# Kernel optimization log

Hardware: AMD Instinct MI355X
Metric: run time of the kernel (lower is better)

Reference implementation:

```python
import jax, jax.numpy as jnp
import numpy as np

D = 128  # hard-coded hidden dim in MLP_T

def setup_inputs() -> dict:
    key = jax.random.key(0)
    ks = jax.random.split(key, 8)
    N, IN = 16384, 768
    return {
        "x": jax.random.normal(ks[0], (N, IN), dtype=jnp.float32),
        "decay_value": 1,
        "W_token": jax.random.normal(ks[1], (IN, D), dtype=jnp.float32) * (IN ** -0.5),
        "b_token": jax.random.normal(ks[2], (D,), dtype=jnp.float32) * 0.02,
        "W_qkv": jax.random.normal(ks[3], (D, 3 * D), dtype=jnp.float32) * (D ** -0.5),
        "b_qkv": jax.random.normal(ks[4], (3 * D,), dtype=jnp.float32) * 0.02,
        "W_fc": jax.random.normal(ks[5], (D, 1), dtype=jnp.float32) * (D ** -0.5),
        "b_fc": jax.random.normal(ks[6], (1,), dtype=jnp.float32) * 0.02,
    }

def reference(x, decay_value, W_token, b_token, W_qkv, b_qkv, W_fc, b_fc):
    # token projection: [N, in_chan] -> [N, 128]
    h = x @ W_token + b_token
    # qkv: [N, 384] split along feature dim into q, k, v of [N, 128]
    qkv = h @ W_qkv + b_qkv
    q, k, v = qkv[:, :D], qkv[:, D:2 * D], qkv[:, 2 * D:]
    # sigmoid attention (no row normalization); dropout is identity in eval mode
    att_scores = jax.nn.sigmoid(q @ k.T)            # [N, N]
    att = att_scores @ v                            # [N, 128]
    out = att @ W_fc + b_fc                         # [N, 1]
    # GradientReversal is identity in the forward pass
    return out
```

## Files before the change

kernel.cpp:

```cpp
#include <hip/hip_runtime.h>
#include <hip/hip_bf16.h>
#include <stdint.h>

#define N_ROWS 16384

typedef __bf16 bf16x8 __attribute__((ext_vector_type(8)));
typedef float f32x4 __attribute__((ext_vector_type(4)));

#define AS1 __attribute__((address_space(1)))
#define AS3 __attribute__((address_space(3)))

#define OFF_WCS  0u
#define OFF_BC   589824u
#define OFF_QB   591360u
#define OFF_KB   4785664u
#define OFF_WV   8979968u

__global__ void prep(const float* __restrict__ Wt, const float* __restrict__ Wq,
                     const float* __restrict__ bt, const float* __restrict__ bq,
                     __bf16* __restrict__ WcS, float* __restrict__ bc) {
    int u = blockIdx.x * 256 + threadIdx.x;
    if (u < 768 * 96) {
        int k = u / 96, n4 = u % 96;
        float s[4] = {0, 0, 0, 0};
        const float* wtp = Wt + k * 128;
        const float* wqp = Wq + n4 * 4;
#pragma unroll 8
        for (int d = 0; d < 128; d++) {
            float a = wtp[d];
            float4 b = *(const float4*)(wqp + d * 384);
            s[0] += a * b.x; s[1] += a * b.y; s[2] += a * b.z; s[3] += a * b.w;
        }
        int kb_ = k >> 6, c = (k >> 3) & 7, k7 = k & 7;
#pragma unroll
        for (int j = 0; j < 4; j++) {
            int n = n4 * 4 + j;
            WcS[n * 768 + kb_ * 64 + ((c ^ (n & 7)) << 3) + k7] = (__bf16)s[j];
        }
    }
    if (u < 384) {
        float s = bq[u];
        for (int d = 0; d < 128; d++) s += bt[d] * Wq[d * 384 + u];
        bc[u] = s;
    }
}

__launch_bounds__(256)
__global__ void gemm_qkv(const float* __restrict__ x, const __bf16* __restrict__ WcS,
                         const float* __restrict__ bc, const float* __restrict__ W_fc,
                         const float* __restrict__ b_fc,
                         __bf16* __restrict__ qb, __bf16* __restrict__ kb,
                         float* __restrict__ wv, float* __restrict__ out) {
    __shared__ float  Asm_[64 * 64];
    __shared__ __bf16 Bsm[128 * 64];
    __shared__ float  wred[64];
    const int tid = threadIdx.x, wave = tid >> 6, lane = tid & 63;
    const int n16 = lane & 15, q = lane >> 4;
    const int mh = wave >> 1, nw = wave & 1;
    const int row0 = blockIdx.x * 64;
    const int sp = blockIdx.y;

    if (sp == 2 && tid < 64) out[row0 + tid] = b_fc[0];

    const char* aptr[4];
    const char* bptr[4];
    {
        int p = (lane & 15) >> 1, half = lane & 1;
#pragma unroll
        for (int i = 0; i < 4; i++) {
            int ar = row0 + wave * 16 + i * 4 + (lane >> 4);
            aptr[i] = (const char*)x + (size_t)ar * 3072 + ((p ^ (ar & 7)) * 8 + half * 4) * 4;
            int br = sp * 128 + wave * 32 + i * 8 + (lane >> 3);
            bptr[i] = (const char*)WcS + (size_t)br * 1536 + (lane & 7) * 16;
        }
    }
    f32x4 acc[2][4];
#pragma unroll
    for (int mt = 0; mt < 2; mt++)
#pragma unroll
        for (int t = 0; t < 4; t++) acc[mt][t] = (f32x4){0, 0, 0, 0};

    for (int kbi = 0; kbi < 12; kbi++) {
#pragma unroll
        for (int i = 0; i < 4; i++)
            __builtin_amdgcn_global_load_lds((const AS1 void*)(aptr[i] + kbi * 256),
                (AS3 void*)((char*)Asm_ + wave * 4096 + i * 1024), 16, 0, 0);
#pragma unroll
        for (int i = 0; i < 4; i++)
            __builtin_amdgcn_global_load_lds((const AS1 void*)(bptr[i] + kbi * 128),
                (AS3 void*)((char*)Bsm + wave * 4096 + i * 1024), 16, 0, 0);
        __syncthreads();
#pragma unroll
        for (int ks = 0; ks < 2; ks++) {
            const int P = ks * 4 + q;
            bf16x8 af[2];
#pragma unroll
            for (int mt = 0; mt < 2; mt++) {
                const int r = mh * 32 + mt * 16 + n16;
                const int sa = r & 7;
                const float* ap = Asm_ + r * 64 + ((P ^ sa) << 3);
                f32x4 f0 = *(const f32x4*)ap;
                f32x4 f1 = *(const f32x4*)(ap + 4);
                bf16x8 t;
                t[0] = (__bf16)f0[0]; t[1] = (__bf16)f0[1]; t[2] = (__bf16)f0[2]; t[3] = (__bf16)f0[3];
                t[4] = (__bf16)f1[0]; t[5] = (__bf16)f1[1]; t[6] = (__bf16)f1[2]; t[7] = (__bf16)f1[3];
                af[mt] = t;
            }
#pragma unroll
            for (int t = 0; t < 4; t++) {
                const int swz = (P ^ (n16 & 7)) << 3;
                bf16x8 bf = *(const bf16x8*)(Bsm + (nw * 64 + t * 16 + n16) * 64 + swz);
                acc[0][t] = __builtin_amdgcn_mfma_f32_16x16x32_bf16(af[0], bf, acc[0][t], 0, 0, 0);
                acc[1][t] = __builtin_amdgcn_mfma_f32_16x16x32_bf16(af[1], bf, acc[1][t], 0, 0, 0);
            }
        }
        __syncthreads();
    }

    const int clb = nw * 64 + n16;
    if (sp == 0) {
#pragma unroll
        for (int t = 0; t < 4; t++) {
            int cl = clb + t * 16;
            float bcv = bc[cl];
#pragma unroll
            for (int mt = 0; mt < 2; mt++)
#pragma unroll
                for (int r = 0; r < 4; r++) {
                    int row = row0 + mh * 32 + mt * 16 + q * 4 + r;
                    qb[row * 128 + cl] = (__bf16)((acc[mt][t][r] + bcv) * -1.44269504088896f);
                }
        }
    } else if (sp == 1) {
#pragma unroll
        for (int t = 0; t < 4; t++) {
            int d = clb + t * 16;
            float bcv = bc[128 + d];
#pragma unroll
            for (int mt = 0; mt < 2; mt++)
#pragma unroll
                for (int r = 0; r < 4; r++) {
                    int row = row0 + mh * 32 + mt * 16 + q * 4 + r;
                    kb[row * 128 + d] = (__bf16)(acc[mt][t][r] + bcv);
                }
        }
    } else {
        float wacc[2][4] = {{0, 0, 0, 0}, {0, 0, 0, 0}};
#pragma unroll
        for (int t = 0; t < 4; t++) {
            int cl = clb + t * 16;
            float bcv = bc[256 + cl];
            float wf = W_fc[cl];
#pragma unroll
            for (int mt = 0; mt < 2; mt++)
#pragma unroll
                for (int r = 0; r < 4; r++) wacc[mt][r] += (acc[mt][t][r] + bcv) * wf;
        }
        float vred[2][4];
#pragma unroll
        for (int mt = 0; mt < 2; mt++)
#pragma unroll
            for (int r = 0; r < 4; r++) {
                float v = wacc[mt][r];
                v += __shfl_xor(v, 1, 64);
                v += __shfl_xor(v, 2, 64);
                v += __shfl_xor(v, 4, 64);
                v += __shfl_xor(v, 8, 64);
                vred[mt][r] = v;
                if (nw == 0 && n16 == 0) wred[mh * 32 + mt * 16 + q * 4 + r] = v;
            }
        __syncthreads();
        if (nw == 1 && n16 == 0) {
#pragma unroll
            for (int mt = 0; mt < 2; mt++)
#pragma unroll
                for (int r = 0; r < 4; r++) {
                    int lr = mh * 32 + mt * 16 + q * 4 + r;
                    wv[row0 + lr] = wred[lr] + vred[mt][r];
                }
        }
    }
}

__launch_bounds__(256, 3)
__global__ void attn(const __bf16* __restrict__ qb, const __bf16* __restrict__ kb,
                     const float* __restrict__ wv, float* __restrict__ out) {
    const int tid = threadIdx.x;
    const int wave = tid >> 6, lane = tid & 63;
    const int n16 = lane & 15, q = lane >> 4;
    const int row0 = blockIdx.x * 256 + wave * 64;
    const int jbase = blockIdx.y * 1024;

    bf16x8 qf[4][4];
#pragma unroll
    for (int mt = 0; mt < 4; mt++)
#pragma unroll
        for (int ks = 0; ks < 4; ks++)
            qf[mt][ks] = *(const bf16x8*)(qb + (row0 + mt * 16 + n16) * 128 + ks * 32 + q * 8);

    float acc[4][4] = {{0}, {0}, {0}, {0}};
    const __bf16* kp = kb + (size_t)(jbase + n16) * 128 + q * 8;
    const float* wp = wv + jbase + n16;

    bf16x8 bcur[4];
    float wcur;
#pragma unroll
    for (int ks = 0; ks < 4; ks++) bcur[ks] = *(const bf16x8*)(kp + ks * 32);
    wcur = wp[0];

#pragma unroll 2
    for (int st = 0; st < 64; st++) {
        bf16x8 bnxt[4];
        const __bf16* kpn = kp + (size_t)(st + 1) * 2048;
#pragma unroll
        for (int ks = 0; ks < 4; ks++) bnxt[ks] = *(const bf16x8*)(kpn + ks * 32);
        float wnxt = wp[(st + 1) * 16];

        f32x4 sc[4];
#pragma unroll
        for (int mt = 0; mt < 4; mt++) sc[mt] = (f32x4){0, 0, 0, 0};
#pragma unroll
        for (int ks = 0; ks < 4; ks++)
#pragma unroll
            for (int mt = 0; mt < 4; mt++)
                sc[mt] = __builtin_amdgcn_mfma_f32_16x16x32_bf16(qf[mt][ks], bcur[ks], sc[mt], 0, 0, 0);
#pragma unroll
        for (int mt = 0; mt < 4; mt++)
#pragma unroll
            for (int r = 0; r < 4; r++)
                acc[mt][r] += __builtin_amdgcn_rcpf(1.0f + __builtin_amdgcn_exp2f(sc[mt][r])) * wcur;
#pragma unroll
        for (int ks = 0; ks < 4; ks++) bcur[ks] = bnxt[ks];
        wcur = wnxt;
    }

#pragma unroll
    for (int mt = 0; mt < 4; mt++)
#pragma unroll
        for (int r = 0; r < 4; r++) {
            float v = acc[mt][r];
            v += __shfl_xor(v, 1, 64);
            v += __shfl_xor(v, 2, 64);
            v += __shfl_xor(v, 4, 64);
            v += __shfl_xor(v, 8, 64);
            if (n16 == 0) atomicAdd(&out[row0 + mt * 16 + q * 4 + r], v);
        }
}

extern "C" void kernel_launch(void* const* d_in, const int* in_sizes, int n_in,
                              void* d_out, int out_size, void* d_ws, size_t ws_size,
                              hipStream_t stream) {
    const float* x       = (const float*)d_in[0];
    const float* W_token = (const float*)d_in[2];
    const float* b_token = (const float*)d_in[3];
    const float* W_qkv   = (const float*)d_in[4];
    const float* b_qkv   = (const float*)d_in[5];
    const float* W_fc    = (const float*)d_in[6];
    const float* b_fc    = (const float*)d_in[7];
    float* out = (float*)d_out;
    char* ws = (char*)d_ws;

    __bf16* WcS = (__bf16*)(ws + OFF_WCS);
    float*  bc  = (float*)(ws + OFF_BC);
    __bf16* qb  = (__bf16*)(ws + OFF_QB);
    __bf16* kb  = (__bf16*)(ws + OFF_KB);
    float*  wv  = (float*)(ws + OFF_WV);

    prep<<<288, 256, 0, stream>>>(W_token, W_qkv, b_token, b_qkv, WcS, bc);
    gemm_qkv<<<dim3(256, 3), 256, 0, stream>>>(x, WcS, bc, W_fc, b_fc, qb, kb, wv, out);
    attn<<<dim3(64, 16), 256, 0, stream>>>(qb, kb, wv, out);
}
```

Baseline: 248.2 us.

## Stage K tiles through LDS with async global_load_lds and swizzled layout

The attention kernel now runs single-wave blocks that copy 64-row K tiles into shared memory with global_load_lds, then read MFMA operands from LDS using an XOR swizzle. The K-writing path of the QKV GEMM stores K in the matching swizzled layout to avoid LDS bank conflicts. The grid changes to 256x8 blocks of 64 threads, each covering a 2048-column slice. This aims to replace per-lane strided global loads of K with coalesced bulk transfers. The cost is a barrier per tile with no double buffering, so loads and compute no longer overlap within a wave.

```diff
diff --git a/kernel.cpp b/kernel.cpp
--- a/kernel.cpp
+++ b/kernel.cpp
@@ -141,7 +141,7 @@
 #pragma unroll
                 for (int r = 0; r < 4; r++) {
                     int row = row0 + mh * 32 + mt * 16 + q * 4 + r;
-                    kb[row * 128 + d] = (__bf16)(acc[mt][t][r] + bcv);
+                    kb[row * 128 + (((d >> 3) ^ (row & 15)) << 3) + (d & 7)] = (__bf16)(acc[mt][t][r] + bcv);
                 }
         }
     } else {
@@ -182,14 +182,15 @@
     }
 }
 
-__launch_bounds__(256, 3)
+__launch_bounds__(64)
 __global__ void attn(const __bf16* __restrict__ qb, const __bf16* __restrict__ kb,
                      const float* __restrict__ wv, float* __restrict__ out) {
-    const int tid = threadIdx.x;
-    const int wave = tid >> 6, lane = tid & 63;
+    __shared__ __bf16 kbuf[64 * 128];
+    __shared__ float wbuf[64];
+    const int lane = threadIdx.x;
     const int n16 = lane & 15, q = lane >> 4;
-    const int row0 = blockIdx.x * 256 + wave * 64;
-    const int jbase = blockIdx.y * 1024;
+    const int row0 = blockIdx.x * 64;
+    const int jslice = blockIdx.y * 2048;
 
     bf16x8 qf[4][4];
 #pragma unroll
@@ -199,41 +200,41 @@
             qf[mt][ks] = *(const bf16x8*)(qb + (row0 + mt * 16 + n16) * 128 + ks * 32 + q * 8);
 
     float acc[4][4] = {{0}, {0}, {0}, {0}};
-    const __bf16* kp = kb + (size_t)(jbase + n16) * 128 + q * 8;
-    const float* wp = wv + jbase + n16;
-
-    bf16x8 bcur[4];
-    float wcur;
-#pragma unroll
-    for (int ks = 0; ks < 4; ks++) bcur[ks] = *(const bf16x8*)(kp + ks * 32);
-    wcur = wp[0];
-
-#pragma unroll 2
-    for (int st = 0; st < 64; st++) {
-        bf16x8 bnxt[4];
-        const __bf16* kpn = kp + (size_t)(st + 1) * 2048;
-#pragma unroll
-        for (int ks = 0; ks < 4; ks++) bnxt[ks] = *(const bf16x8*)(kpn + ks * 32);
-        float wnxt = wp[(st + 1) * 16];
-
-        f32x4 sc[4];
-#pragma unroll
-        for (int mt = 0; mt < 4; mt++) sc[mt] = (f32x4){0, 0, 0, 0};
-#pragma unroll
-        for (int ks = 0; ks < 4; ks++)
+    for (int jc = 0; jc < 32; jc++) {
+        const int jbase = jslice + jc * 64;
+        const char* gsrc = (const char*)kb + (size_t)jbase * 256;
+#pragma unroll
+        for (int i = 0; i < 16; i++)
+            __builtin_amdgcn_global_load_lds(
+                (const AS1 void*)(gsrc + i * 1024 + lane * 16),
+                (AS3 void*)((char*)kbuf + i * 1024), 16, 0, 0);
+        wbuf[lane] = wv[jbase + lane];
+        __syncthreads();
+#pragma unroll
+        for (int t = 0; t < 4; t++) {
+            bf16x8 bf[4];
+#pragma unroll
+            for (int ks = 0; ks < 4; ks++) {
+                const int chunk = (ks * 4 + q) ^ n16;
+                bf[ks] = *(const bf16x8*)(kbuf + (t * 16 + n16) * 128 + chunk * 8);
+            }
+            f32x4 sc[4];
+#pragma unroll
+            for (int mt = 0; mt < 4; mt++) sc[mt] = (f32x4){0, 0, 0, 0};
+#pragma unroll
+            for (int ks = 0; ks < 4; ks++)
+#pragma unroll
+                for (int mt = 0; mt < 4; mt++)
+                    sc[mt] = __builtin_amdgcn_mfma_f32_16x16x32_bf16(qf[mt][ks], bf[ks], sc[mt], 0, 0, 0);
+            const float wval = wbuf[t * 16 + n16];
 #pragma unroll
             for (int mt = 0; mt < 4; mt++)
-                sc[mt] = __builtin_amdgcn_mfma_f32_16x16x32_bf16(qf[mt][ks], bcur[ks], sc[mt], 0, 0, 0);
-#pragma unroll
-        for (int mt = 0; mt < 4; mt++)
-#pragma unroll
-            for (int r = 0; r < 4; r++)
-                acc[mt][r] += __builtin_amdgcn_rcpf(1.0f + __builtin_amdgcn_exp2f(sc[mt][r])) * wcur;
-#pragma unroll
-        for (int ks = 0; ks < 4; ks++) bcur[ks] = bnxt[ks];
-        wcur = wnxt;
-    }
-
+#pragma unroll
+                for (int r = 0; r < 4; r++)
+                    acc[mt][r] += __builtin_amdgcn_rcpf(1.0f + __builtin_amdgcn_exp2f(sc[mt][r])) * wval;
+        }
+        __syncthreads();
+    }
 #pragma unroll
     for (int mt = 0; mt < 4; mt++)
 #pragma unroll
@@ -268,5 +269,5 @@
 
     prep<<<288, 256, 0, stream>>>(W_token, W_qkv, b_token, b_qkv, WcS, bc);
     gemm_qkv<<<dim3(256, 3), 256, 0, stream>>>(x, WcS, bc, W_fc, b_fc, qb, kb, wv, out);
-    attn<<<dim3(64, 16), 256, 0, stream>>>(qb, kb, wv, out);
-}
+    attn<<<dim3(256, 8), 64, 0, stream>>>(qb, kb, wv, out);
+}
```

Result: slower. 253.8 us (+2.3%).
